# Kernel optimization log

Hardware: AMD Instinct MI355X
Metric: run time of the kernel (lower is better)

## Reference

```python
import jax, jax.numpy as jnp
import numpy as np

BN_EPS = 1e-5


def _mlp_layer(x, W, b, gamma, beta):
    # x: [B, N, Cin]; Conv1d(k=1) == per-point linear, then BatchNorm1d over (B,N), ReLU
    y = jnp.einsum('bnc,oc->bno', x, W) + b  # [B, N, Cout]
    mean = y.mean(axis=(0, 1))
    var = y.var(axis=(0, 1))
    y = (y - mean) * jax.lax.rsqrt(var + BN_EPS) * gamma + beta
    return jax.nn.relu(y)


def setup_inputs() -> dict:
    key = jax.random.key(0)
    ks = jax.random.split(key, 12)
    B, N, M, C1, C2 = 4, 16384, 4096, 64, 256
    Cin = C1 + C2  # 320
    H1, H2 = 256, 128
    inp = {
        'xyz_fine': jax.random.normal(ks[0], (B, N, 3), jnp.float32),
        'xyz_coarse': jax.random.normal(ks[1], (B, M, 3), jnp.float32),
        'feats_fine': jax.random.normal(ks[2], (B, N, C1), jnp.float32),
        'feats_coarse': jax.random.normal(ks[3], (B, M, C2), jnp.float32),
        'W1': jax.random.normal(ks[4], (H1, Cin), jnp.float32) * (1.0 / np.sqrt(Cin)),
        'b1': jnp.zeros((H1,), jnp.float32),
        'g1': jnp.ones((H1,), jnp.float32),
        'be1': jnp.zeros((H1,), jnp.float32),
        'W2': jax.random.normal(ks[5], (H2, H1), jnp.float32) * (1.0 / np.sqrt(H1)),
        'b2': jnp.zeros((H2,), jnp.float32),
        'g2': jnp.ones((H2,), jnp.float32),
        'be2': jnp.zeros((H2,), jnp.float32),
    }
    return inp


def reference(xyz_fine, xyz_coarse, feats_fine, feats_coarse,
              W1, b1, g1, be1, W2, b2, g2, be2):
    # squared pairwise distance: [B, N, M]
    d = (jnp.sum(xyz_fine ** 2, -1, keepdims=True)
         - 2.0 * jnp.einsum('bnd,bmd->bnm', xyz_fine, xyz_coarse)
         + jnp.sum(xyz_coarse ** 2, -1)[:, None, :])
    # 3 smallest distances
    neg_d, idx = jax.lax.top_k(-d, 3)        # idx: [B, N, 3]
    dists = jnp.maximum(-neg_d, 1e-10)
    w = 1.0 / dists
    w = w / jnp.sum(w, -1, keepdims=True)    # [B, N, 3]
    # gather coarse features: [B, N, 3, C2]
    gathered = jax.vmap(lambda f, i: f[i])(feats_coarse, idx)
    interp = jnp.einsum('bnk,bnkc->bnc', w, gathered)  # [B, N, C2]
    x = jnp.concatenate([interp, feats_fine], axis=-1)  # [B, N, Cin]
    x = _mlp_layer(x, W1, b1, g1, be1)
    x = _mlp_layer(x, W2, b2, g2, be2)
    return x  # [B, N, 128]
```

## Files before the change

kernel.cpp:

```cpp
#include <hip/hip_runtime.h>
#include <hip/hip_bf16.h>
#include <stdint.h>

#define B_    4
#define N_    16384
#define M_    4096
#define C1_   64
#define C2_   256
#define CIN_  320
#define H1_   256
#define H2_   128
#define ROWS_ (B_*N_)
#define SPLIT_ 8
#define CHUNK_ (M_/SPLIT_)

typedef __attribute__((ext_vector_type(8))) short bf16x8;
typedef __attribute__((ext_vector_type(4))) float f32x4;
typedef __attribute__((ext_vector_type(8))) unsigned short u16x8;
typedef __attribute__((ext_vector_type(4))) unsigned short u16x4;

static __device__ __forceinline__ unsigned short f2bf(float f) {
  union { float f; unsigned u; } v; v.f = f;
  unsigned r = v.u + 0x7fffu + ((v.u >> 16) & 1u);
  return (unsigned short)(r >> 16);
}
static __device__ __forceinline__ float bf2f(unsigned short h) {
  union { unsigned u; float f; } v; v.u = ((unsigned)h) << 16;
  return v.f;
}

static __device__ __forceinline__ void gload16(const void* g, void* lds) {
  __builtin_amdgcn_global_load_lds(
      (__attribute__((address_space(1))) void*)(uintptr_t)g,
      (__attribute__((address_space(3))) void*)(uintptr_t)lds,
      16, 0, 0);
}

#define INS3(dv, iv) do {                                        \
  float _d = (dv); int _ii = (iv);                               \
  if (_d < d3) {                                                 \
    if (_d < d2) {                                               \
      d3 = d2; i3 = i2;                                          \
      if (_d < d1) { d2 = d1; i2 = i1; d1 = _d; i1 = _ii; }      \
      else         { d2 = _d; i2 = _ii; }                        \
    } else { d3 = _d; i3 = _ii; }                                \
  } } while (0)

__global__ __launch_bounds__(256) void prep(
    const float* __restrict__ W1, const float* __restrict__ W2,
    const float* __restrict__ xyzc, const float* __restrict__ fc,
    unsigned short* __restrict__ W1b, unsigned short* __restrict__ W2b,
    float4* __restrict__ cpk, unsigned short* __restrict__ fcb)
{
  int i = blockIdx.x * 256 + threadIdx.x;
  if (i < H1_*CIN_) W1b[i] = f2bf(W1[i]);
  if (i < H2_*H1_)  W2b[i] = f2bf(W2[i]);
  if (i < B_*M_) {
    float x = xyzc[i*3], y = xyzc[i*3+1], z = xyzc[i*3+2];
    cpk[i] = make_float4(x, y, z, x*x + y*y + z*z);
  }
  const int total4 = B_*M_*C2_/4;
  const int stride = gridDim.x * 256;
  for (int t = i; t < total4; t += stride) {
    float4 v = ((const float4*)fc)[t];
    u16x4 o;
    o[0] = f2bf(v.x); o[1] = f2bf(v.y); o[2] = f2bf(v.z); o[3] = f2bf(v.w);
    ((u16x4*)fcb)[t] = o;
  }
}

__global__ __launch_bounds__(256) void nn_scan(
    const float* __restrict__ xyzf, const float4* __restrict__ cpk,
    float4* __restrict__ pdw, int4* __restrict__ piw)
{
  __shared__ float4 cp[CHUNK_];
  const int tid  = threadIdx.x;
  const int s    = blockIdx.x & (SPLIT_-1);
  const int tile = (blockIdx.x >> 3) & 63;
  const int b    = blockIdx.x >> 9;

  const float4* src = cpk + (size_t)b * M_ + s * CHUNK_;
  for (int i = tid; i < CHUNK_; i += 256) cp[i] = src[i];
  __syncthreads();

  const int p = tile * 256 + tid;
  const size_t gp = (size_t)b * N_ + p;
  const float* xf = xyzf + gp * 3;
  const float fx = xf[0], fy = xf[1], fz = xf[2];
  const float xx = fx*fx + fy*fy + fz*fz;
  const float nx = -2.f*fx, ny = -2.f*fy, nz = -2.f*fz;

  float d1 = 3.4e38f, d2 = 3.4e38f, d3 = 3.4e38f;
  int   i1 = 0, i2 = 0, i3 = 0;

  #pragma unroll 1
  for (int g = 0; g < CHUNK_; g += 8) {
    float dd[8];
    #pragma unroll
    for (int u = 0; u < 8; ++u) {
      float4 c = cp[g + u];
      dd[u] = xx + fmaf(nx, c.x, fmaf(ny, c.y, fmaf(nz, c.z, c.w)));
    }
    #pragma unroll
    for (int u = 0; u < 8; ++u) {
      float d = dd[u]; int j = g + u;
      if (d < d3) {
        bool c1 = d < d1, c2 = d < d2;
        d3 = c2 ? d2 : d;              i3 = c2 ? i2 : j;
        d2 = c1 ? d1 : (c2 ? d : d2);  i2 = c1 ? i1 : (c2 ? j : i2);
        d1 = c1 ? d  : d1;             i1 = c1 ? j  : i1;
      }
    }
  }
  const int base = s * CHUNK_;
  pdw[(size_t)s * ROWS_ + gp] = make_float4(d1, d2, d3, 0.f);
  piw[(size_t)s * ROWS_ + gp] = make_int4(i1 + base, i2 + base, i3 + base, 0);
}

__global__ __launch_bounds__(256) void nn_finish(
    const float4* __restrict__ pdw, const int4* __restrict__ piw,
    const float* __restrict__ ff, const unsigned short* __restrict__ fcb,
    unsigned short* __restrict__ X)
{
  __shared__ float wv[64][3];
  __shared__ int   wi[64][3];
  const int tid  = threadIdx.x;
  const int b    = blockIdx.x >> 8;
  const int tile = blockIdx.x & 255;
  const size_t gp0 = (size_t)b * N_ + tile * 64;

  if (tid < 64) {
    const size_t gp = gp0 + tid;
    float d1 = 3.4e38f, d2 = 3.4e38f, d3 = 3.4e38f;
    int   i1 = 0, i2 = 0, i3 = 0;
    #pragma unroll
    for (int s = 0; s < SPLIT_; ++s) {
      float4 dv = pdw[(size_t)s * ROWS_ + gp];
      int4   iv = piw[(size_t)s * ROWS_ + gp];
      INS3(dv.x, iv.x);
      INS3(dv.y, iv.y);
      INS3(dv.z, iv.z);
    }
    d1 = fmaxf(d1, 1e-10f); d2 = fmaxf(d2, 1e-10f); d3 = fmaxf(d3, 1e-10f);
    float u1 = 1.f/d1, u2 = 1.f/d2, u3 = 1.f/d3;
    float inv = 1.f/(u1 + u2 + u3);
    wv[tid][0] = u1*inv; wv[tid][1] = u2*inv; wv[tid][2] = u3*inv;
    wi[tid][0] = i1;     wi[tid][1] = i2;     wi[tid][2] = i3;
  }
  __syncthreads();

  const int w = tid >> 6, l = tid & 63;
  const unsigned short* fcb_b = fcb + (size_t)b * M_ * C2_;
  unsigned short* Xb = X + gp0 * CIN_;
  #pragma unroll 2
  for (int q = 0; q < 16; ++q) {
    int pl = w * 16 + q;
    float a1 = wv[pl][0], a2 = wv[pl][1], a3 = wv[pl][2];
    int   j1 = wi[pl][0], j2 = wi[pl][1], j3 = wi[pl][2];
    u16x4 r1 = ((const u16x4*)(fcb_b + (size_t)j1 * C2_))[l];
    u16x4 r2 = ((const u16x4*)(fcb_b + (size_t)j2 * C2_))[l];
    u16x4 r3 = ((const u16x4*)(fcb_b + (size_t)j3 * C2_))[l];
    u16x4 o;
    #pragma unroll
    for (int e = 0; e < 4; ++e) {
      float v = fmaf(a1, bf2f(r1[e]), fmaf(a2, bf2f(r2[e]), a3 * bf2f(r3[e])));
      o[e] = f2bf(v);
    }
    *(u16x4*)(Xb + (size_t)pl * CIN_ + l * 4) = o;
  }

  {
    const float* ffb = ff + gp0 * C1_;
    int pl = tid >> 2, c0 = (tid & 3) * 16;
    const float4* fsrc = (const float4*)(ffb + (size_t)pl * C1_ + c0);
    unsigned short* dst = Xb + (size_t)pl * CIN_ + C2_ + c0;
    #pragma unroll
    for (int t = 0; t < 4; ++t) {
      float4 v = fsrc[t];
      u16x4 o;
      o[0] = f2bf(v.x); o[1] = f2bf(v.y); o[2] = f2bf(v.z); o[3] = f2bf(v.w);
      *(u16x4*)(dst + t * 4) = o;
    }
  }
}

template<int K, int NTOT, bool OUTBF>
__global__ __launch_bounds__(256) void gemm_stats(
    const unsigned short* __restrict__ A,
    const unsigned short* __restrict__ Bw,
    unsigned short* __restrict__ Yb,
    float* __restrict__ Yf,
    float* __restrict__ part)
{
  constexpr int BM = 128, BN = 128, BK = 64;
  constexpr int NCT = NTOT / BN;
  __shared__ unsigned short As[BM*BK];
  __shared__ unsigned short Bs[BN*BK];
  __shared__ float sred[2][BN][2];

  const int tid = threadIdx.x;
  const int l   = tid & 63;
  const int w   = tid >> 6;
  const int wm  = w >> 1, wn = w & 1;
  const int rt  = blockIdx.x / NCT, ct = blockIdx.x % NCT;
  const int lr  = l & 15;
  const int lk  = (l >> 4) * 8;

  const unsigned short* Arow = A  + (size_t)rt * BM * K;
  const unsigned short* Brow = Bw + (size_t)ct * BN * K;

  f32x4 acc[4][4] = {};

  for (int k0 = 0; k0 < K; k0 += BK) {
    #pragma unroll
    for (int q = 0; q < 4; ++q) {
      int chunk = q * 256 + tid;
      int row = chunk >> 3, cc = chunk & 7;
      unsigned ldsoff = (unsigned)(q * 256 + (tid & ~63)) * 16u;
      gload16(Arow + (size_t)row * K + k0 + cc * 8, (char*)As + ldsoff);
      gload16(Brow + (size_t)row * K + k0 + cc * 8, (char*)Bs + ldsoff);
    }
    __syncthreads();
    #pragma unroll
    for (int kk = 0; kk < BK/32; ++kk) {
      bf16x8 af[4], bfr[4];
      #pragma unroll
      for (int m = 0; m < 4; ++m)
        af[m] = *(const bf16x8*)(As + (wm*64 + m*16 + lr)*BK + kk*32 + lk);
      #pragma unroll
      for (int n = 0; n < 4; ++n)
        bfr[n] = *(const bf16x8*)(Bs + (wn*64 + n*16 + lr)*BK + kk*32 + lk);
      #pragma unroll
      for (int m = 0; m < 4; ++m)
        #pragma unroll
        for (int n = 0; n < 4; ++n)
          acc[m][n] = __builtin_amdgcn_mfma_f32_16x16x32_bf16(af[m], bfr[n], acc[m][n], 0, 0, 0);
    }
    __syncthreads();
  }

  const int orow0 = rt*BM + wm*64;
  const int ocol0 = ct*BN + wn*64;
  #pragma unroll
  for (int n = 0; n < 4; ++n) {
    float s = 0.f, qq = 0.f;
    #pragma unroll
    for (int m = 0; m < 4; ++m) {
      #pragma unroll
      for (int r = 0; r < 4; ++r) {
        float v = acc[m][n][r];
        int row = orow0 + m*16 + (l >> 4)*4 + r;
        int col = ocol0 + n*16 + lr;
        size_t off = (size_t)row * NTOT + col;
        if (OUTBF) Yb[off] = f2bf(v); else Yf[off] = v;
        s += v; qq += v*v;
      }
    }
    s  += __shfl_xor(s, 16);  s  += __shfl_xor(s, 32);
    qq += __shfl_xor(qq, 16); qq += __shfl_xor(qq, 32);
    if (l < 16) {
      sred[wm][wn*64 + n*16 + l][0] = s;
      sred[wm][wn*64 + n*16 + l][1] = qq;
    }
  }
  __syncthreads();
  if (tid < BN) {
    float S = sred[0][tid][0] + sred[1][tid][0];
    float Q = sred[0][tid][1] + sred[1][tid][1];
    part[((size_t)rt * NTOT + ct*BN + tid) * 2 + 0] = S;
    part[((size_t)rt * NTOT + ct*BN + tid) * 2 + 1] = Q;
  }
}

template<int K, int NTOT>
__global__ __launch_bounds__(256) void gemm_bnrelu_stats(
    const unsigned short* __restrict__ Yin,
    const float* __restrict__ ab,
    const unsigned short* __restrict__ Bw,
    float* __restrict__ Yf,
    float* __restrict__ part)
{
  constexpr int BM = 128, BN = 128, BK = 64;
  constexpr int NCT = NTOT / BN;
  __shared__ unsigned short As[BM*BK];
  __shared__ unsigned short Bs[BN*BK];
  __shared__ float sa[K], sb[K];
  __shared__ float sred[2][BN][2];

  const int tid = threadIdx.x;
  const int l   = tid & 63;
  const int w   = tid >> 6;
  const int wm  = w >> 1, wn = w & 1;
  const int rt  = blockIdx.x / NCT, ct = blockIdx.x % NCT;
  const int lr  = l & 15;
  const int lk  = (l >> 4) * 8;
  const int cc  = tid & 7;
  const int r0  = tid >> 3;

  sa[tid] = ab[tid*2];
  sb[tid] = ab[tid*2 + 1];

  const unsigned short* Arow = Yin + (size_t)rt * BM * K;
  const unsigned short* Brow = Bw  + (size_t)ct * BN * K;

  f32x4 acc[4][4] = {};
  __syncthreads();

  for (int k0 = 0; k0 < K; k0 += BK) {
    #pragma unroll
    for (int q = 0; q < 4; ++q) {
      int chunk = q * 256 + tid;
      int row = chunk >> 3, c8 = chunk & 7;
      unsigned ldsoff = (unsigned)(q * 256 + (tid & ~63)) * 16u;
      gload16(Brow + (size_t)row * K + k0 + c8 * 8, (char*)Bs + ldsoff);
    }
    float a_[8], b_[8];
    *(float4*)&a_[0] = *(const float4*)&sa[k0 + cc*8];
    *(float4*)&a_[4] = *(const float4*)&sa[k0 + cc*8 + 4];
    *(float4*)&b_[0] = *(const float4*)&sb[k0 + cc*8];
    *(float4*)&b_[4] = *(const float4*)&sb[k0 + cc*8 + 4];
    #pragma unroll
    for (int q = 0; q < 4; ++q) {
      int row = q*32 + r0;
      u16x8 v = *(const u16x8*)(Arow + (size_t)row * K + k0 + cc*8);
      u16x8 o;
      #pragma unroll
      for (int e = 0; e < 8; ++e) {
        float f = fmaxf(fmaf(bf2f((unsigned short)v[e]), a_[e], b_[e]), 0.f);
        o[e] = f2bf(f);
      }
      *(u16x8*)((char*)As + (unsigned)(q*256 + tid) * 16u) = o;
    }
    __syncthreads();
    #pragma unroll
    for (int kk = 0; kk < BK/32; ++kk) {
      bf16x8 af[4], bfr[4];
      #pragma unroll
      for (int m = 0; m < 4; ++m)
        af[m] = *(const bf16x8*)(As + (wm*64 + m*16 + lr)*BK + kk*32 + lk);
      #pragma unroll
      for (int n = 0; n < 4; ++n)
        bfr[n] = *(const bf16x8*)(Bs + (wn*64 + n*16 + lr)*BK + kk*32 + lk);
      #pragma unroll
      for (int m = 0; m < 4; ++m)
        #pragma unroll
        for (int n = 0; n < 4; ++n)
          acc[m][n] = __builtin_amdgcn_mfma_f32_16x16x32_bf16(af[m], bfr[n], acc[m][n], 0, 0, 0);
    }
    __syncthreads();
  }

  const int orow0 = rt*BM + wm*64;
  const int ocol0 = ct*BN + wn*64;
  #pragma unroll
  for (int n = 0; n < 4; ++n) {
    float s = 0.f, qq = 0.f;
    #pragma unroll
    for (int m = 0; m < 4; ++m) {
      #pragma unroll
      for (int r = 0; r < 4; ++r) {
        float v = acc[m][n][r];
        int row = orow0 + m*16 + (l >> 4)*4 + r;
        int col = ocol0 + n*16 + lr;
        Yf[(size_t)row * NTOT + col] = v;
        s += v; qq += v*v;
      }
    }
    s  += __shfl_xor(s, 16);  s  += __shfl_xor(s, 32);
    qq += __shfl_xor(qq, 16); qq += __shfl_xor(qq, 32);
    if (l < 16) {
      sred[wm][wn*64 + n*16 + l][0] = s;
      sred[wm][wn*64 + n*16 + l][1] = qq;
    }
  }
  __syncthreads();
  if (tid < BN) {
    float S = sred[0][tid][0] + sred[1][tid][0];
    float Q = sred[0][tid][1] + sred[1][tid][1];
    part[((size_t)rt * NTOT + ct*BN + tid) * 2 + 0] = S;
    part[((size_t)rt * NTOT + ct*BN + tid) * 2 + 1] = Q;
  }
}

__global__ void finalize_stats(const float* __restrict__ part,
                               const float* __restrict__ g,
                               const float* __restrict__ be,
                               float* __restrict__ ab, int nrt, int C, float invM)
{
  const int c = blockIdx.x;
  const int t = threadIdx.x;
  float s = 0.f, q = 0.f;
  for (int r = t; r < nrt; r += 64) {
    s += part[((size_t)r * C + c) * 2 + 0];
    q += part[((size_t)r * C + c) * 2 + 1];
  }
  #pragma unroll
  for (int o = 32; o > 0; o >>= 1) { s += __shfl_down(s, o); q += __shfl_down(q, o); }
  if (t == 0) {
    float mean = s * invM;
    float var  = q * invM - mean * mean;
    float rstd = rsqrtf(var + 1e-5f);
    float a = g[c] * rstd;
    ab[c*2 + 0] = a;
    ab[c*2 + 1] = be[c] - mean * a;
  }
}

__global__ __launch_bounds__(256) void bnrelu_out(
    const float* __restrict__ Y, const float* __restrict__ ab,
    float* __restrict__ out)
{
  __shared__ float sa[H2_], sb[H2_];
  if (threadIdx.x < H2_) { sa[threadIdx.x] = ab[threadIdx.x*2]; sb[threadIdx.x] = ab[threadIdx.x*2+1]; }
  __syncthreads();
  const size_t total = (size_t)ROWS_ * H2_ / 4;
  for (size_t i = (size_t)blockIdx.x*256 + threadIdx.x; i < total; i += (size_t)gridDim.x*256) {
    float4 v = ((const float4*)Y)[i];
    int cb = (int)((i * 4) & (H2_ - 1));
    float4 o;
    o.x = fmaxf(fmaf(v.x, sa[cb+0], sb[cb+0]), 0.f);
    o.y = fmaxf(fmaf(v.y, sa[cb+1], sb[cb+1]), 0.f);
    o.z = fmaxf(fmaf(v.z, sa[cb+2], sb[cb+2]), 0.f);
    o.w = fmaxf(fmaf(v.w, sa[cb+3], sb[cb+3]), 0.f);
    ((float4*)out)[i] = o;
  }
}

extern "C" void kernel_launch(void* const* d_in, const int* in_sizes, int n_in,
                              void* d_out, int out_size, void* d_ws, size_t ws_size,
                              hipStream_t stream)
{
  const float* xyzf = (const float*)d_in[0];
  const float* xyzc = (const float*)d_in[1];
  const float* ff   = (const float*)d_in[2];
  const float* fc   = (const float*)d_in[3];
  const float* W1   = (const float*)d_in[4];
  const float* g1   = (const float*)d_in[6];
  const float* be1  = (const float*)d_in[7];
  const float* W2   = (const float*)d_in[8];
  const float* g2   = (const float*)d_in[10];
  const float* be2  = (const float*)d_in[11];
  float* out = (float*)d_out;

  char* ws = (char*)d_ws;
  unsigned short* W1b  = (unsigned short*)(ws + 0);
  unsigned short* W2b  = (unsigned short*)(ws + 163840);
  unsigned short* X    = (unsigned short*)(ws + 229376);
  float*          Y2   = (float*)         (ws + 229376);
  unsigned short* fcb  = (unsigned short*)(ws + 42172416);
  unsigned short* Y1   = (unsigned short*)(ws + 42172416);
  float* part1 = (float*)(ws + 75726848);
  float* part2 = (float*)(ws + 76775424);
  float* ab1   = (float*)(ws + 77299712);
  float* ab2   = (float*)(ws + 77301760);
  float4* cpk  = (float4*)(ws + 77302784);
  float4* pdw  = (float4*)(ws + 77564928);
  int4*   piw  = (int4*)  (ws + 85953536);

  prep<<<1024, 256, 0, stream>>>(W1, W2, xyzc, fc, W1b, W2b, cpk, fcb);
  nn_scan<<<B_ * 64 * SPLIT_, 256, 0, stream>>>(xyzf, cpk, pdw, piw);
  nn_finish<<<B_ * 256, 256, 0, stream>>>(pdw, piw, ff, fcb, X);

  gemm_stats<CIN_, H1_, true><<<(ROWS_/128) * (H1_/128), 256, 0, stream>>>(
      X, W1b, Y1, nullptr, part1);
  finalize_stats<<<H1_, 64, 0, stream>>>(part1, g1, be1, ab1, ROWS_/128, H1_, 1.f/ROWS_);

  gemm_bnrelu_stats<H1_, H2_><<<(ROWS_/128) * (H2_/128), 256, 0, stream>>>(
      Y1, ab1, W2b, Y2, part2);
  finalize_stats<<<H2_, 64, 0, stream>>>(part2, g2, be2, ab2, ROWS_/128, H2_, 1.f/ROWS_);
  bnrelu_out<<<2048, 256, 0, stream>>>(Y2, ab2, out);
}
```

Measured before the change: 169.4 us.

## Branchless top-3 insert, grouped GEMM block order, bf16 layer-2 intermediate

The nearest-neighbour scan drops the per-point |x|^2 add from the inner loop, adding it once at the end, and replaces the branchy top-3 insertion with a branchless sorting network to avoid divergence. The first GEMM remaps block indices so the two column tiles of neighbouring row tiles run together, which should improve cache reuse of the A tiles. The second GEMM stores its pre-BN output as bf16 instead of fp32, halving the intermediate write and read in the final BN+ReLU pass. That pass is rewritten to read 8 bf16 values per thread. The bf16 intermediate adds rounding error to the output, and the branchless insert does more selects per candidate.

```diff
diff --git a/kernel.cpp b/kernel.cpp
--- a/kernel.cpp
+++ b/kernel.cpp
@@ -99,21 +99,23 @@
     #pragma unroll
     for (int u = 0; u < 8; ++u) {
       float4 c = cp[g + u];
-      dd[u] = xx + fmaf(nx, c.x, fmaf(ny, c.y, fmaf(nz, c.z, c.w)));
+      dd[u] = fmaf(nx, c.x, fmaf(ny, c.y, fmaf(nz, c.z, c.w)));
     }
     #pragma unroll
     for (int u = 0; u < 8; ++u) {
       float d = dd[u]; int j = g + u;
-      if (d < d3) {
-        bool c1 = d < d1, c2 = d < d2;
-        d3 = c2 ? d2 : d;              i3 = c2 ? i2 : j;
-        d2 = c1 ? d1 : (c2 ? d : d2);  i2 = c1 ? i1 : (c2 ? j : i2);
-        d1 = c1 ? d  : d1;             i1 = c1 ? j  : i1;
-      }
+      bool c1 = d < d1;
+      float h1d = c1 ? d1 : d;   int h1i = c1 ? i1 : j;
+      d1       = c1 ? d  : d1;   i1      = c1 ? j  : i1;
+      bool c2 = h1d < d2;
+      float h2d = c2 ? d2  : h1d; int h2i = c2 ? i2  : h1i;
+      d2       = c2 ? h1d : d2;   i2      = c2 ? h1i : i2;
+      bool c3 = h2d < d3;
+      d3 = c3 ? h2d : d3;         i3 = c3 ? h2i : i3;
     }
   }
   const int base = s * CHUNK_;
-  pdw[(size_t)s * ROWS_ + gp] = make_float4(d1, d2, d3, 0.f);
+  pdw[(size_t)s * ROWS_ + gp] = make_float4(d1 + xx, d2 + xx, d3 + xx, 0.f);
   piw[(size_t)s * ROWS_ + gp] = make_int4(i1 + base, i2 + base, i3 + base, 0);
 }
 
@@ -202,7 +204,13 @@
   const int l   = tid & 63;
   const int w   = tid >> 6;
   const int wm  = w >> 1, wn = w & 1;
-  const int rt  = blockIdx.x / NCT, ct = blockIdx.x % NCT;
+  int rt, ct;
+  if (NCT == 2) {
+    rt = (blockIdx.x & 7) | ((blockIdx.x >> 4) << 3);
+    ct = (blockIdx.x >> 3) & 1;
+  } else {
+    rt = blockIdx.x / NCT; ct = blockIdx.x % NCT;
+  }
   const int lr  = l & 15;
   const int lk  = (l >> 4) * 8;
 
@@ -277,7 +285,7 @@
     const unsigned short* __restrict__ Yin,
     const float* __restrict__ ab,
     const unsigned short* __restrict__ Bw,
-    float* __restrict__ Yf,
+    unsigned short* __restrict__ Yb,
     float* __restrict__ part)
 {
   constexpr int BM = 128, BN = 128, BK = 64;
@@ -362,7 +370,7 @@
         float v = acc[m][n][r];
         int row = orow0 + m*16 + (l >> 4)*4 + r;
         int col = ocol0 + n*16 + lr;
-        Yf[(size_t)row * NTOT + col] = v;
+        Yb[(size_t)row * NTOT + col] = f2bf(v);
         s += v; qq += v*v;
       }
     }
@@ -407,22 +415,27 @@
 }
 
 __global__ __launch_bounds__(256) void bnrelu_out(
-    const float* __restrict__ Y, const float* __restrict__ ab,
+    const unsigned short* __restrict__ Y, const float* __restrict__ ab,
     float* __restrict__ out)
 {
   __shared__ float sa[H2_], sb[H2_];
   if (threadIdx.x < H2_) { sa[threadIdx.x] = ab[threadIdx.x*2]; sb[threadIdx.x] = ab[threadIdx.x*2+1]; }
   __syncthreads();
-  const size_t total = (size_t)ROWS_ * H2_ / 4;
+  const size_t total = (size_t)ROWS_ * H2_ / 8;
   for (size_t i = (size_t)blockIdx.x*256 + threadIdx.x; i < total; i += (size_t)gridDim.x*256) {
-    float4 v = ((const float4*)Y)[i];
-    int cb = (int)((i * 4) & (H2_ - 1));
-    float4 o;
-    o.x = fmaxf(fmaf(v.x, sa[cb+0], sb[cb+0]), 0.f);
-    o.y = fmaxf(fmaf(v.y, sa[cb+1], sb[cb+1]), 0.f);
-    o.z = fmaxf(fmaf(v.z, sa[cb+2], sb[cb+2]), 0.f);
-    o.w = fmaxf(fmaf(v.w, sa[cb+3], sb[cb+3]), 0.f);
-    ((float4*)out)[i] = o;
+    u16x8 v = ((const u16x8*)Y)[i];
+    int cb = (int)((i * 8) & (H2_ - 1));
+    float4 o0, o1;
+    o0.x = fmaxf(fmaf(bf2f((unsigned short)v[0]), sa[cb+0], sb[cb+0]), 0.f);
+    o0.y = fmaxf(fmaf(bf2f((unsigned short)v[1]), sa[cb+1], sb[cb+1]), 0.f);
+    o0.z = fmaxf(fmaf(bf2f((unsigned short)v[2]), sa[cb+2], sb[cb+2]), 0.f);
+    o0.w = fmaxf(fmaf(bf2f((unsigned short)v[3]), sa[cb+3], sb[cb+3]), 0.f);
+    o1.x = fmaxf(fmaf(bf2f((unsigned short)v[4]), sa[cb+4], sb[cb+4]), 0.f);
+    o1.y = fmaxf(fmaf(bf2f((unsigned short)v[5]), sa[cb+5], sb[cb+5]), 0.f);
+    o1.z = fmaxf(fmaf(bf2f((unsigned short)v[6]), sa[cb+6], sb[cb+6]), 0.f);
+    o1.w = fmaxf(fmaf(bf2f((unsigned short)v[7]), sa[cb+7], sb[cb+7]), 0.f);
+    ((float4*)out)[i*2]   = o0;
+    ((float4*)out)[i*2+1] = o1;
   }
 }
 
@@ -446,7 +459,7 @@
   unsigned short* W1b  = (unsigned short*)(ws + 0);
   unsigned short* W2b  = (unsigned short*)(ws + 163840);
   unsigned short* X    = (unsigned short*)(ws + 229376);
-  float*          Y2   = (float*)         (ws + 229376);
+  unsigned short* Y2b  = (unsigned short*)(ws + 229376);
   unsigned short* fcb  = (unsigned short*)(ws + 42172416);
   unsigned short* Y1   = (unsigned short*)(ws + 42172416);
   float* part1 = (float*)(ws + 75726848);
@@ -466,7 +479,7 @@
   finalize_stats<<<H1_, 64, 0, stream>>>(part1, g1, be1, ab1, ROWS_/128, H1_, 1.f/ROWS_);
 
   gemm_bnrelu_stats<H1_, H2_><<<(ROWS_/128) * (H2_/128), 256, 0, stream>>>(
-      Y1, ab1, W2b, Y2, part2);
+      Y1, ab1, W2b, Y2b, part2);
   finalize_stats<<<H2_, 64, 0, stream>>>(part2, g2, be2, ab2, ROWS_/128, H2_, 1.f/ROWS_);
-  bnrelu_out<<<2048, 256, 0, stream>>>(Y2, ab2, out);
-}
+  bnrelu_out<<<2048, 256, 0, stream>>>(Y2b, ab2, out);
+}
```

Result: slower. 190.7 us (+12.6%).
